# Performance work log

Measured on AMD Instinct MI355X. Metric: run time of the kernel, lower is better.

The kernel has to match this reference:

```python
import jax, jax.numpy as jnp
import numpy as np

E = 512   # embed_dim
H = 16    # num_heads
D = E // H  # head_dim = 32
L = 2048  # target (query) length
S = 2048  # source (stored pattern) length
N = 4     # batch
LN_EPS = 1e-5


def setup_inputs() -> dict:
    key = jax.random.key(0)
    ks = jax.random.split(key, 8)
    inv_sqrt_e = 1.0 / np.sqrt(E).astype(np.float32)
    return {
        "query": jax.random.normal(ks[0], (L, N, E), jnp.float32),
        "key_in": jax.random.normal(ks[1], (S, N, E), jnp.float32),
        "value": jax.random.normal(ks[2], (S, N, E), jnp.float32),
        "scaling": jax.random.uniform(ks[3], (H,), jnp.float32),  # per-head beta
        "in_proj_weight": jax.random.normal(ks[4], (3 * E, E), jnp.float32) * inv_sqrt_e,
        "in_proj_bias": jnp.zeros((3 * E,), jnp.float32),
        "p_norm_weight": jnp.ones((D,), jnp.float32),
        "p_norm_bias": jnp.zeros((D,), jnp.float32),
        "out_proj_weight": jax.random.normal(ks[5], (E, E), jnp.float32) * inv_sqrt_e,
        "out_proj_bias": jnp.zeros((E,), jnp.float32),
    }


def reference(query, key_in, value, scaling, in_proj_weight, in_proj_bias,
              p_norm_weight, p_norm_bias, out_proj_weight, out_proj_bias):
    Lq, Nb, Ed = query.shape
    Sk = key_in.shape[0]
    # split packed in-projection (torch Linear convention: y = x @ W^T + b)
    wq, wk, wv = jnp.split(in_proj_weight, 3, axis=0)
    bq, bk, bv = jnp.split(in_proj_bias, 3, axis=0)
    q = jnp.einsum('lne,fe->lnf', query, wq) + bq
    k = jnp.einsum('sne,fe->snf', key_in, wk) + bk
    v = jnp.einsum('sne,fe->snf', value, wv) + bv
    # (len, N, H*D) -> (N, H, len, D)
    q = q.reshape(Lq, Nb, H, D).transpose(1, 2, 0, 3)
    k = k.reshape(Sk, Nb, H, D).transpose(1, 2, 0, 3)
    v = v.reshape(Sk, Nb, H, D).transpose(1, 2, 0, 3)

    def pattern_norm(x):
        # affine LayerNorm over the association (head) dimension D
        mu = jnp.mean(x, axis=-1, keepdims=True)
        var = jnp.mean(jnp.square(x - mu), axis=-1, keepdims=True)
        return (x - mu) * jax.lax.rsqrt(var + LN_EPS) * p_norm_weight + p_norm_bias

    k = pattern_norm(k)
    v = pattern_norm(v)

    beta = scaling.reshape(1, H, 1, 1)  # per-head inverse-temperature
    scores = jnp.einsum('nhld,nhsd->nhls', q * beta, k)  # [N,H,L,S]
    attn = jax.nn.softmax(scores, axis=-1)  # single Hopfield update (update_steps_max=0)
    out = jnp.einsum('nhls,nhsd->nhld', attn, v)  # [N,H,L,D]
    out = out.transpose(2, 0, 1, 3).reshape(Lq, Nb, H * D)
    out = jnp.einsum('lnf,of->lno', out, out_proj_weight) + out_proj_bias
    return out  # (L, N, E)
```

## Files before the change

kernel.cpp:

```cpp
#include <hip/hip_runtime.h>
#include <cstdint>

#define LN_EPS 1e-5f

typedef _Float16 f16;
typedef _Float16 half4_t __attribute__((ext_vector_type(4)));
typedef _Float16 half8_t __attribute__((ext_vector_type(8)));
typedef __fp16 fp16v2 __attribute__((ext_vector_type(2)));
typedef float f32x4 __attribute__((ext_vector_type(4)));

__device__ __forceinline__ void gl_lds16(const void* g, void* l) {
    __builtin_amdgcn_global_load_lds(
        (__attribute__((address_space(1))) void*)(uintptr_t)g,
        (__attribute__((address_space(3))) void*)(uint32_t)(uintptr_t)l,
        16, 0, 0);
}

__device__ __forceinline__ half4_t pack4(float a, float b, float c, float d) {
    fp16v2 lo = __builtin_amdgcn_cvt_pkrtz(a, b);
    fp16v2 hi = __builtin_amdgcn_cvt_pkrtz(c, d);
    half4_t r;
    r[0] = (f16)lo[0]; r[1] = (f16)lo[1]; r[2] = (f16)hi[0]; r[3] = (f16)hi[1];
    return r;
}

__global__ void k_cast(const float* __restrict__ W1f, const float* __restrict__ W2f,
                       const float* __restrict__ Xq, const float* __restrict__ Xk,
                       const float* __restrict__ Xv,
                       f16* __restrict__ W1h, f16* __restrict__ W2h,
                       f16* __restrict__ Xh) {
    int t = blockIdx.x * blockDim.x + threadIdx.x;
    const float4* src;
    half4_t* dst;
    int idx;
    if (t < 196608)      { src = (const float4*)W1f; dst = (half4_t*)W1h; idx = t; }
    else if (t < 262144) { src = (const float4*)W2f; dst = (half4_t*)W2h; idx = t - 196608; }
    else {
        int u = t - 262144;
        int s = u >> 20;
        idx = u & 1048575;
        src = (s == 0) ? (const float4*)Xq : ((s == 1) ? (const float4*)Xk : (const float4*)Xv);
        dst = (half4_t*)(Xh + (size_t)s * 4194304);
    }
    float4 v = src[idx];
    dst[idx] = pack4(v.x, v.y, v.z, v.w);
}

__global__ __launch_bounds__(256) void k_inproj(
    const f16* __restrict__ Xh, const f16* __restrict__ W1,
    const float* __restrict__ bias, const float* __restrict__ scaling,
    f16* __restrict__ Qg, f16* __restrict__ Kg, f16* __restrict__ Vg)
{
    __shared__ __align__(16) f16 Al[128 * 32];
    __shared__ __align__(16) f16 Bl[128 * 32];

    const int tid = threadIdx.x;
    const int m0 = blockIdx.x * 128;
    const int f0 = blockIdx.y * 128;
    const int sec = f0 >> 9;
    const f16* X = Xh + (size_t)sec * 4194304;
    f16* Ob = (sec == 0) ? Qg : ((sec == 1) ? Kg : Vg);

    const int wid = tid >> 6, ln = tid & 63, l15 = ln & 15, quad = ln >> 4;
    const int wm = wid >> 1, wn = wid & 1;

    f32x4 z4 = {0.f, 0.f, 0.f, 0.f};
    f32x4 acc[4][4];
    #pragma unroll
    for (int i = 0; i < 4; ++i)
        #pragma unroll
        for (int j = 0; j < 4; ++j) acc[i][j] = z4;

    for (int kt = 0; kt < 16; ++kt) {
        const int k0 = kt * 32;
        #pragma unroll
        for (int i = 0; i < 2; ++i) {
            int row = wid * 32 + i * 16 + (ln >> 2);
            int co = (ln & 3) * 8;
            gl_lds16(W1 + (size_t)(f0 + row) * 512 + k0 + co,
                     Bl + (wid * 32 + i * 16) * 32);
            gl_lds16(X + (size_t)(m0 + row) * 512 + k0 + co,
                     Al + (wid * 32 + i * 16) * 32);
        }
        __syncthreads();

        half8_t a[4], b[4];
        #pragma unroll
        for (int i = 0; i < 4; ++i)
            a[i] = *(const half8_t*)(Al + (wm * 64 + i * 16 + l15) * 32 + quad * 8);
        #pragma unroll
        for (int j = 0; j < 4; ++j)
            b[j] = *(const half8_t*)(Bl + (wn * 64 + j * 16 + l15) * 32 + quad * 8);
        #pragma unroll
        for (int i = 0; i < 4; ++i)
            #pragma unroll
            for (int j = 0; j < 4; ++j)
                acc[i][j] = __builtin_amdgcn_mfma_f32_16x16x32_f16(b[j], a[i], acc[i][j], 0, 0, 0);
        __syncthreads();
    }

    #pragma unroll
    for (int j = 0; j < 4; ++j) {
        int fb = f0 + wn * 64 + j * 16;
        int floc = (fb & 511) + quad * 4;
        int hh = floc >> 5;
        int cc = (floc >> 3) & 3, e0 = floc & 7;
        float sc2 = (sec == 0) ? scaling[hh] * 1.44269504f : 1.0f;
        float4 bs4 = *(const float4*)(bias + fb + quad * 4);
        #pragma unroll
        for (int i = 0; i < 4; ++i) {
            int rm = m0 + wm * 64 + i * 16 + l15;
            int l = rm >> 2, nb = rm & 3;
            int gg = nb * 16 + hh;
            *(half4_t*)(Ob + (size_t)gg * 65536 + (size_t)cc * 16384 + (size_t)l * 8 + e0) =
                pack4((acc[i][j][0] + bs4.x) * sc2, (acc[i][j][1] + bs4.y) * sc2,
                      (acc[i][j][2] + bs4.z) * sc2, (acc[i][j][3] + bs4.w) * sc2);
        }
    }
}

__global__ void k_norm_kv(f16* __restrict__ Kg, const f16* __restrict__ Vg,
                          const float* __restrict__ w, const float* __restrict__ b,
                          f16* __restrict__ Vtg) {
    __shared__ __align__(16) f16 T[32 * 64];
    const int t = threadIdx.x;
    const int seg = blockIdx.x, g = blockIdx.y;
    const int s_l = t >> 2, c = t & 3;
    const size_t base = (size_t)g * 65536 + (size_t)c * 16384 + (size_t)(seg * 64 + s_l) * 8;

    half8_t kv = *(const half8_t*)(Kg + base);
    half8_t vv = *(const half8_t*)(Vg + base);
    float kf[8], vf[8];
    float ks1 = 0.f, ks2 = 0.f, vs1 = 0.f, vs2 = 0.f;
    #pragma unroll
    for (int j = 0; j < 8; ++j) {
        kf[j] = (float)kv[j]; ks1 += kf[j]; ks2 += kf[j] * kf[j];
        vf[j] = (float)vv[j]; vs1 += vf[j]; vs2 += vf[j] * vf[j];
    }
    ks1 += __shfl_xor(ks1, 1); ks1 += __shfl_xor(ks1, 2);
    ks2 += __shfl_xor(ks2, 1); ks2 += __shfl_xor(ks2, 2);
    vs1 += __shfl_xor(vs1, 1); vs1 += __shfl_xor(vs1, 2);
    vs2 += __shfl_xor(vs2, 1); vs2 += __shfl_xor(vs2, 2);
    float kmu = ks1 * (1.f / 32.f), kvar = ks2 * (1.f / 32.f) - kmu * kmu;
    float vmu = vs1 * (1.f / 32.f), vvar = vs2 * (1.f / 32.f) - vmu * vmu;
    float krs = rsqrtf(kvar + LN_EPS), vrs = rsqrtf(vvar + LN_EPS);

    half8_t ky;
    int cs = s_l >> 3, es = s_l & 7;
    #pragma unroll
    for (int j = 0; j < 8; ++j) {
        int d = c * 8 + j;
        float wd = w[d], bd = b[d];
        ky[j] = (f16)((kf[j] - kmu) * krs * wd + bd);
        T[d * 64 + (cs ^ j) * 8 + es] = (f16)((vf[j] - vmu) * vrs * wd + bd);
    }
    *(half8_t*)(Kg + base) = ky;
    __syncthreads();
    int d_o = t >> 3, c_o = t & 7;
    half8_t out = *(const half8_t*)(T + d_o * 64 + c_o * 8);
    *(half8_t*)(Vtg + (size_t)(g * 32 + seg) * 2048 + d_o * 64 + c_o * 8) = out;
}

__global__ __launch_bounds__(256, 4) void k_flash(
    const f16* __restrict__ Qg, const f16* __restrict__ Kg,
    const f16* __restrict__ Vtg, f16* __restrict__ Og)
{
    __shared__ __align__(16) char smem[40960];

    const int tid = threadIdx.x, wid = tid >> 6, ln = tid & 63;
    const int l15 = ln & 15, quad = ln >> 4, l8 = ln & 7;
    char* Pw = smem + 24576 + wid * 4096;
    const int g = blockIdx.x, h = g & 15, n = g >> 4;
    const int q0 = blockIdx.y * 128;

    half8_t aq[2];
    #pragma unroll
    for (int i = 0; i < 2; ++i)
        aq[i] = *(const half8_t*)(Qg + (size_t)g * 65536 + (size_t)quad * 16384 +
                                  (size_t)(q0 + wid * 32 + i * 16 + l15) * 8);

    const f16* kp = Kg + (size_t)g * 65536 + (size_t)wid * 16384;
    const f16* vp = Vtg + (size_t)(g * 32) * 2048 + wid * 512;
    gl_lds16(kp + (size_t)ln * 8, smem + wid * 1024);
    gl_lds16(vp + (size_t)ln * 8, smem + 12288 + wid * 1024);
    gl_lds16(kp + 512 + (size_t)ln * 8, smem + 4096 + wid * 1024);
    gl_lds16(vp + 2048 + (size_t)ln * 8, smem + 12288 + 4096 + wid * 1024);
    kp += 1024;
    vp += 4096;

    half8_t onesf;
    {
        f16 o = (l15 == 0) ? (f16)1.0f : (f16)0.0f;
        #pragma unroll
        for (int j = 0; j < 8; ++j) onesf[j] = o;
    }

    f32x4 z4 = {0.f, 0.f, 0.f, 0.f};
    f32x4 accO[2][2], accSum[2];
    accO[0][0] = z4; accO[0][1] = z4; accO[1][0] = z4; accO[1][1] = z4;
    accSum[0] = z4; accSum[1] = z4;
    float m_i[2] = {-1e30f, -1e30f};

    int cur = 0;
    for (int st = 0; st < 32; ++st) {
        if (st < 31) asm volatile("s_waitcnt vmcnt(2)" ::: "memory");
        else         asm volatile("s_waitcnt vmcnt(0)" ::: "memory");
        __builtin_amdgcn_s_barrier();

        if (st < 30) {
            int nb = cur + 2; if (nb >= 3) nb -= 3;
            gl_lds16(kp + (size_t)ln * 8, smem + nb * 4096 + wid * 1024);
            gl_lds16(vp + (size_t)ln * 8, smem + 12288 + nb * 4096 + wid * 1024);
            kp += 512;
            vp += 2048;
        }
        const char* Kl = smem + cur * 4096;
        const char* Vt = smem + 12288 + cur * 4096;

        half8_t ak[4];
        #pragma unroll
        for (int mt = 0; mt < 4; ++mt)
            ak[mt] = *(const half8_t*)(Kl + quad * 1024 + (mt * 16 + l15) * 16);
        f32x4 accS[2][4];
        __builtin_amdgcn_s_setprio(1);
        #pragma unroll
        for (int i = 0; i < 2; ++i)
            #pragma unroll
            for (int mt = 0; mt < 4; ++mt)
                accS[i][mt] = __builtin_amdgcn_mfma_f32_16x16x32_f16(ak[mt], aq[i], z4, 0, 0, 0);
        __builtin_amdgcn_s_setprio(0);

        float mn[2];
        bool up = false;
        #pragma unroll
        for (int i = 0; i < 2; ++i) {
            float xm = fmaxf(fmaxf(accS[i][0][0], accS[i][0][1]),
                             fmaxf(accS[i][0][2], accS[i][0][3]));
            #pragma unroll
            for (int mt = 1; mt < 4; ++mt)
                xm = fmaxf(xm, fmaxf(fmaxf(accS[i][mt][0], accS[i][mt][1]),
                                     fmaxf(accS[i][mt][2], accS[i][mt][3])));
            xm = fmaxf(xm, __shfl_xor(xm, 16));
            xm = fmaxf(xm, __shfl_xor(xm, 32));
            up = up || (xm > m_i[i] + 8.f);
            mn[i] = fmaxf(m_i[i], xm);
        }
        if (__ballot(up)) {
            #pragma unroll
            for (int i = 0; i < 2; ++i) {
                float alpha = __builtin_amdgcn_exp2f(m_i[i] - mn[i]);
                #pragma unroll
                for (int dt = 0; dt < 2; ++dt)
                    #pragma unroll
                    for (int r = 0; r < 4; ++r) accO[i][dt][r] *= alpha;
                #pragma unroll
                for (int r = 0; r < 4; ++r) accSum[i][r] *= alpha;
                m_i[i] = mn[i];
            }
        }

        #pragma unroll
        for (int i = 0; i < 2; ++i) {
            #pragma unroll
            for (int mt = 0; mt < 4; ++mt) {
                float p0 = __builtin_amdgcn_exp2f(accS[i][mt][0] - m_i[i]);
                float p1 = __builtin_amdgcn_exp2f(accS[i][mt][1] - m_i[i]);
                float p2 = __builtin_amdgcn_exp2f(accS[i][mt][2] - m_i[i]);
                float p3 = __builtin_amdgcn_exp2f(accS[i][mt][3] - m_i[i]);
                int ch = (mt * 2 + (quad >> 1)) ^ l8;
                *(half4_t*)(Pw + (i * 16 + l15) * 128 + ch * 16 + (quad & 1) * 8) =
                    pack4(p0, p1, p2, p3);
            }
        }

        #pragma unroll
        for (int kt = 0; kt < 2; ++kt) {
            half8_t av[2], bp[2];
            #pragma unroll
            for (int dt = 0; dt < 2; ++dt) {
                int d = dt * 16 + l15;
                int cp = (kt * 4 + quad) ^ (l15 & 7);
                av[dt] = *(const half8_t*)(Vt + d * 128 + cp * 16);
            }
            #pragma unroll
            for (int i = 0; i < 2; ++i)
                bp[i] = *(const half8_t*)(Pw + (i * 16 + l15) * 128 +
                                          (((kt * 4 + quad) ^ l8) * 16));
            __builtin_amdgcn_s_setprio(1);
            #pragma unroll
            for (int i = 0; i < 2; ++i) {
                #pragma unroll
                for (int dt = 0; dt < 2; ++dt)
                    accO[i][dt] = __builtin_amdgcn_mfma_f32_16x16x32_f16(av[dt], bp[i], accO[i][dt], 0, 0, 0);
                accSum[i] = __builtin_amdgcn_mfma_f32_16x16x32_f16(onesf, bp[i], accSum[i], 0, 0, 0);
            }
            __builtin_amdgcn_s_setprio(0);
        }

        cur = cur + 1; if (cur == 3) cur = 0;
    }

    #pragma unroll
    for (int i = 0; i < 2; ++i) {
        float li = __shfl(accSum[i][0], l15);
        float inv = 1.f / li;
        #pragma unroll
        for (int dt = 0; dt < 2; ++dt)
            *(half4_t*)(Pw + (i * 16 + l15) * 80 + (dt * 16 + quad * 4) * 2) =
                pack4(accO[i][dt][0] * inv, accO[i][dt][1] * inv,
                      accO[i][dt][2] * inv, accO[i][dt][3] * inv);
    }
    int q2 = ln >> 1, hf = ln & 1;
    half8_t o0 = *(const half8_t*)(Pw + q2 * 80 + hf * 32);
    half8_t o1 = *(const half8_t*)(Pw + q2 * 80 + hf * 32 + 16);
    size_t rowe = ((size_t)(n * 2048 + q0 + wid * 32 + q2)) * 512 + h * 32 + hf * 16;
    *(half8_t*)(Og + rowe) = o0;
    *(half8_t*)(Og + rowe + 8) = o1;
}

__global__ __launch_bounds__(256) void k_outproj(
    const f16* __restrict__ A, const f16* __restrict__ W2,
    const float* __restrict__ bias, float* __restrict__ Out)
{
    __shared__ __align__(16) f16 Al[128 * 32];
    __shared__ __align__(16) f16 Bl[128 * 32];

    const int tid = threadIdx.x;
    const int m0 = blockIdx.x * 128;
    const int f0 = blockIdx.y * 128;
    const int wid = tid >> 6, ln = tid & 63, l15 = ln & 15, quad = ln >> 4;
    const int wm = wid >> 1, wn = wid & 1;

    f32x4 z4 = {0.f, 0.f, 0.f, 0.f};
    f32x4 acc[4][4];
    #pragma unroll
    for (int i = 0; i < 4; ++i)
        #pragma unroll
        for (int j = 0; j < 4; ++j) acc[i][j] = z4;

    for (int kt = 0; kt < 16; ++kt) {
        const int k0 = kt * 32;
        #pragma unroll
        for (int i = 0; i < 2; ++i) {
            int row = wid * 32 + i * 16 + (ln >> 2);
            gl_lds16(A + (size_t)(m0 + row) * 512 + k0 + (ln & 3) * 8,
                     Al + (wid * 32 + i * 16) * 32);
            gl_lds16(W2 + (size_t)(f0 + row) * 512 + k0 + (ln & 3) * 8,
                     Bl + (wid * 32 + i * 16) * 32);
        }
        __syncthreads();

        half8_t a[4], b[4];
        #pragma unroll
        for (int i = 0; i < 4; ++i)
            a[i] = *(const half8_t*)(Al + (wm * 64 + i * 16 + l15) * 32 + quad * 8);
        #pragma unroll
        for (int j = 0; j < 4; ++j)
            b[j] = *(const half8_t*)(Bl + (wn * 64 + j * 16 + l15) * 32 + quad * 8);
        #pragma unroll
        for (int i = 0; i < 4; ++i)
            #pragma unroll
            for (int j = 0; j < 4; ++j)
                acc[i][j] = __builtin_amdgcn_mfma_f32_16x16x32_f16(b[j], a[i], acc[i][j], 0, 0, 0);
        __syncthreads();
    }

    #pragma unroll
    for (int j = 0; j < 4; ++j) {
        int fb = f0 + wn * 64 + j * 16;
        float4 bs4 = *(const float4*)(bias + fb + quad * 4);
        #pragma unroll
        for (int i = 0; i < 4; ++i) {
            int rm = m0 + wm * 64 + i * 16 + l15;
            int orow = (rm & 2047) * 4 + (rm >> 11);
            float4 o;
            o.x = acc[i][j][0] + bs4.x;
            o.y = acc[i][j][1] + bs4.y;
            o.z = acc[i][j][2] + bs4.z;
            o.w = acc[i][j][3] + bs4.w;
            *(float4*)(Out + (size_t)orow * 512 + fb + quad * 4) = o;
        }
    }
}

extern "C" void kernel_launch(void* const* d_in, const int* in_sizes, int n_in,
                              void* d_out, int out_size, void* d_ws, size_t ws_size,
                              hipStream_t stream) {
    const float* query   = (const float*)d_in[0];
    const float* key_in  = (const float*)d_in[1];
    const float* value   = (const float*)d_in[2];
    const float* scaling = (const float*)d_in[3];
    const float* ipw     = (const float*)d_in[4];
    const float* ipb     = (const float*)d_in[5];
    const float* pnw     = (const float*)d_in[6];
    const float* pnb     = (const float*)d_in[7];
    const float* opw     = (const float*)d_in[8];
    const float* opb     = (const float*)d_in[9];
    float* out = (float*)d_out;

    f16* Qg  = (f16*)d_ws;
    f16* Kg  = Qg + (size_t)4194304;
    f16* Vg  = Qg + (size_t)8388608;
    f16* W1  = Qg + (size_t)12582912;
    f16* W2  = Qg + (size_t)13369344;
    f16* Xh  = Qg + (size_t)13631488;
    f16* Vtg = Xh;
    f16* Og  = Vg;

    k_cast<<<13312, 256, 0, stream>>>(ipw, opw, query, key_in, value, W1, W2, Xh);
    k_inproj<<<dim3(64, 12), 256, 0, stream>>>(Xh, W1, ipb, scaling, Qg, Kg, Vg);
    k_norm_kv<<<dim3(32, 64), 256, 0, stream>>>(Kg, Vg, pnw, pnb, Vtg);
    k_flash<<<dim3(64, 16), 256, 0, stream>>>(Qg, Kg, Vtg, Og);
    k_outproj<<<dim3(64, 4), 256, 0, stream>>>(Og, W2, opb, out);
}
```

Baseline: 220.7 us.

## Software-pipeline QK^T one tile ahead of softmax and PV in flash loop

Restructures the flash-attention main loop so the score MFMAs for the next K tile are issued before the softmax and PV work of the current tile. Two score register sets ping-pong through a manually unrolled pair of loop bodies, and the wait count is tightened to match. Occupancy is lowered from 4 to 3 blocks per SM to make room for the extra live accumulators. The aim is to overlap MFMA latency with exp/softmax VALU work, at the cost of more registers and fewer resident waves.

```diff
diff --git a/kernel.cpp b/kernel.cpp
--- a/kernel.cpp
+++ b/kernel.cpp
@@ -161,7 +161,7 @@
     *(half8_t*)(Vtg + (size_t)(g * 32 + seg) * 2048 + d_o * 64 + c_o * 8) = out;
 }
 
-__global__ __launch_bounds__(256, 4) void k_flash(
+__global__ __launch_bounds__(256, 3) void k_flash(
     const f16* __restrict__ Qg, const f16* __restrict__ Kg,
     const f16* __restrict__ Vtg, f16* __restrict__ Og)
 {
@@ -172,12 +172,6 @@
     char* Pw = smem + 24576 + wid * 4096;
     const int g = blockIdx.x, h = g & 15, n = g >> 4;
     const int q0 = blockIdx.y * 128;
-
-    half8_t aq[2];
-    #pragma unroll
-    for (int i = 0; i < 2; ++i)
-        aq[i] = *(const half8_t*)(Qg + (size_t)g * 65536 + (size_t)quad * 16384 +
-                                  (size_t)(q0 + wid * 32 + i * 16 + l15) * 8);
 
     const f16* kp = Kg + (size_t)g * 65536 + (size_t)wid * 16384;
     const f16* vp = Vtg + (size_t)(g * 32) * 2048 + wid * 512;
@@ -188,6 +182,12 @@
     kp += 1024;
     vp += 4096;
 
+    half8_t aq[2];
+    #pragma unroll
+    for (int i = 0; i < 2; ++i)
+        aq[i] = *(const half8_t*)(Qg + (size_t)g * 65536 + (size_t)quad * 16384 +
+                                  (size_t)(q0 + wid * 32 + i * 16 + l15) * 8);
+
     half8_t onesf;
     {
         f16 o = (l15 == 0) ? (f16)1.0f : (f16)0.0f;
@@ -201,45 +201,62 @@
     accSum[0] = z4; accSum[1] = z4;
     float m_i[2] = {-1e30f, -1e30f};
 
+    asm volatile("s_waitcnt vmcnt(0)" ::: "memory");
+    __builtin_amdgcn_s_barrier();
+
+    f32x4 S0[2][4], S1[2][4];
+    {
+        half8_t ak[4];
+        #pragma unroll
+        for (int mt = 0; mt < 4; ++mt)
+            ak[mt] = *(const half8_t*)(smem + quad * 1024 + (mt * 16 + l15) * 16);
+        #pragma unroll
+        for (int i = 0; i < 2; ++i)
+            #pragma unroll
+            for (int mt = 0; mt < 4; ++mt)
+                S0[i][mt] = __builtin_amdgcn_mfma_f32_16x16x32_f16(ak[mt], aq[i], z4, 0, 0, 0);
+    }
+
     int cur = 0;
-    for (int st = 0; st < 32; ++st) {
-        if (st < 31) asm volatile("s_waitcnt vmcnt(2)" ::: "memory");
+    auto body = [&](f32x4 (&SC)[2][4], f32x4 (&SN)[2][4], int st) {
+        if (st < 31) asm volatile("s_waitcnt vmcnt(1)" ::: "memory");
         else         asm volatile("s_waitcnt vmcnt(0)" ::: "memory");
         __builtin_amdgcn_s_barrier();
 
-        if (st < 30) {
+        if (st <= 29) {
             int nb = cur + 2; if (nb >= 3) nb -= 3;
             gl_lds16(kp + (size_t)ln * 8, smem + nb * 4096 + wid * 1024);
             gl_lds16(vp + (size_t)ln * 8, smem + 12288 + nb * 4096 + wid * 1024);
             kp += 512;
             vp += 2048;
         }
-        const char* Kl = smem + cur * 4096;
-        const char* Vt = smem + 12288 + cur * 4096;
-
-        half8_t ak[4];
-        #pragma unroll
-        for (int mt = 0; mt < 4; ++mt)
-            ak[mt] = *(const half8_t*)(Kl + quad * 1024 + (mt * 16 + l15) * 16);
-        f32x4 accS[2][4];
-        __builtin_amdgcn_s_setprio(1);
-        #pragma unroll
-        for (int i = 0; i < 2; ++i)
+
+        if (st <= 30) {
+            int nx = cur + 1; if (nx >= 3) nx -= 3;
+            const char* Kn = smem + nx * 4096;
+            half8_t ak[4];
             #pragma unroll
             for (int mt = 0; mt < 4; ++mt)
-                accS[i][mt] = __builtin_amdgcn_mfma_f32_16x16x32_f16(ak[mt], aq[i], z4, 0, 0, 0);
-        __builtin_amdgcn_s_setprio(0);
+                ak[mt] = *(const half8_t*)(Kn + quad * 1024 + (mt * 16 + l15) * 16);
+            __builtin_amdgcn_s_setprio(1);
+            #pragma unroll
+            for (int i = 0; i < 2; ++i)
+                #pragma unroll
+                for (int mt = 0; mt < 4; ++mt)
+                    SN[i][mt] = __builtin_amdgcn_mfma_f32_16x16x32_f16(ak[mt], aq[i], z4, 0, 0, 0);
+            __builtin_amdgcn_s_setprio(0);
+        }
 
         float mn[2];
         bool up = false;
         #pragma unroll
         for (int i = 0; i < 2; ++i) {
-            float xm = fmaxf(fmaxf(accS[i][0][0], accS[i][0][1]),
-                             fmaxf(accS[i][0][2], accS[i][0][3]));
+            float xm = fmaxf(fmaxf(SC[i][0][0], SC[i][0][1]),
+                             fmaxf(SC[i][0][2], SC[i][0][3]));
             #pragma unroll
             for (int mt = 1; mt < 4; ++mt)
-                xm = fmaxf(xm, fmaxf(fmaxf(accS[i][mt][0], accS[i][mt][1]),
-                                     fmaxf(accS[i][mt][2], accS[i][mt][3])));
+                xm = fmaxf(xm, fmaxf(fmaxf(SC[i][mt][0], SC[i][mt][1]),
+                                     fmaxf(SC[i][mt][2], SC[i][mt][3])));
             xm = fmaxf(xm, __shfl_xor(xm, 16));
             xm = fmaxf(xm, __shfl_xor(xm, 32));
             up = up || (xm > m_i[i] + 8.f);
@@ -263,16 +280,17 @@
         for (int i = 0; i < 2; ++i) {
             #pragma unroll
             for (int mt = 0; mt < 4; ++mt) {
-                float p0 = __builtin_amdgcn_exp2f(accS[i][mt][0] - m_i[i]);
-                float p1 = __builtin_amdgcn_exp2f(accS[i][mt][1] - m_i[i]);
-                float p2 = __builtin_amdgcn_exp2f(accS[i][mt][2] - m_i[i]);
-                float p3 = __builtin_amdgcn_exp2f(accS[i][mt][3] - m_i[i]);
+                float p0 = __builtin_amdgcn_exp2f(SC[i][mt][0] - m_i[i]);
+                float p1 = __builtin_amdgcn_exp2f(SC[i][mt][1] - m_i[i]);
+                float p2 = __builtin_amdgcn_exp2f(SC[i][mt][2] - m_i[i]);
+                float p3 = __builtin_amdgcn_exp2f(SC[i][mt][3] - m_i[i]);
                 int ch = (mt * 2 + (quad >> 1)) ^ l8;
                 *(half4_t*)(Pw + (i * 16 + l15) * 128 + ch * 16 + (quad & 1) * 8) =
                     pack4(p0, p1, p2, p3);
             }
         }
 
+        const char* Vt = smem + 12288 + cur * 4096;
         #pragma unroll
         for (int kt = 0; kt < 2; ++kt) {
             half8_t av[2], bp[2];
@@ -298,6 +316,11 @@
         }
 
         cur = cur + 1; if (cur == 3) cur = 0;
+    };
+
+    for (int it = 0; it < 16; ++it) {
+        body(S0, S1, it * 2);
+        body(S1, S0, it * 2 + 1);
     }
 
     #pragma unroll
```

Result: slower. 232.7 us (+5.4%).

## Triple-buffer LDS loads in projection GEMMs and halve outproj M tile

Applied to the files above, without the earlier changes.

Both projection GEMMs now use a three-slot LDS ring with async global-to-LDS loads issued two k-steps ahead. Explicit vmcnt waits and a single barrier per iteration replace the two __syncthreads, and s_setprio is raised around the MFMA block so memory latency overlaps with compute. The output projection also shrinks its M tile from 128 to 64 rows, doubling its grid to 512 blocks so more CUs are busy. The cost is more LDS per block and reliance on hand-counted vmcnt values, which are fragile if the compiler reorders or adds memory ops.

```diff
diff --git a/kernel.cpp b/kernel.cpp
--- a/kernel.cpp
+++ b/kernel.cpp
@@ -51,8 +51,8 @@
     const float* __restrict__ bias, const float* __restrict__ scaling,
     f16* __restrict__ Qg, f16* __restrict__ Kg, f16* __restrict__ Vg)
 {
-    __shared__ __align__(16) f16 Al[128 * 32];
-    __shared__ __align__(16) f16 Bl[128 * 32];
+    __shared__ __align__(16) f16 Al[3][128 * 32];
+    __shared__ __align__(16) f16 Bl[3][128 * 32];
 
     const int tid = threadIdx.x;
     const int m0 = blockIdx.x * 128;
@@ -63,6 +63,7 @@
 
     const int wid = tid >> 6, ln = tid & 63, l15 = ln & 15, quad = ln >> 4;
     const int wm = wid >> 1, wn = wid & 1;
+    const int srow = ln >> 2, sco = (ln & 3) * 8;
 
     f32x4 z4 = {0.f, 0.f, 0.f, 0.f};
     f32x4 acc[4][4];
@@ -71,32 +72,47 @@
         #pragma unroll
         for (int j = 0; j < 4; ++j) acc[i][j] = z4;
 
+    auto issue = [&](int kt, int slot) {
+        const int k0 = kt * 32;
+        #pragma unroll
+        for (int i = 0; i < 2; ++i) {
+            int row = wid * 32 + i * 16 + srow;
+            gl_lds16(W1 + (size_t)(f0 + row) * 512 + k0 + sco,
+                     Bl[slot] + (wid * 32 + i * 16) * 32);
+            gl_lds16(X + (size_t)(m0 + row) * 512 + k0 + sco,
+                     Al[slot] + (wid * 32 + i * 16) * 32);
+        }
+    };
+    issue(0, 0);
+    issue(1, 1);
+
+    int slot = 0;
     for (int kt = 0; kt < 16; ++kt) {
-        const int k0 = kt * 32;
-        #pragma unroll
-        for (int i = 0; i < 2; ++i) {
-            int row = wid * 32 + i * 16 + (ln >> 2);
-            int co = (ln & 3) * 8;
-            gl_lds16(W1 + (size_t)(f0 + row) * 512 + k0 + co,
-                     Bl + (wid * 32 + i * 16) * 32);
-            gl_lds16(X + (size_t)(m0 + row) * 512 + k0 + co,
-                     Al + (wid * 32 + i * 16) * 32);
-        }
-        __syncthreads();
+        if (kt < 15) asm volatile("s_waitcnt vmcnt(4)" ::: "memory");
+        else         asm volatile("s_waitcnt vmcnt(0)" ::: "memory");
+        __builtin_amdgcn_s_barrier();
+
+        if (kt < 14) {
+            int nb = slot + 2; if (nb >= 3) nb -= 3;
+            issue(kt + 2, nb);
+        }
 
         half8_t a[4], b[4];
         #pragma unroll
         for (int i = 0; i < 4; ++i)
-            a[i] = *(const half8_t*)(Al + (wm * 64 + i * 16 + l15) * 32 + quad * 8);
+            a[i] = *(const half8_t*)(Al[slot] + (wm * 64 + i * 16 + l15) * 32 + quad * 8);
         #pragma unroll
         for (int j = 0; j < 4; ++j)
-            b[j] = *(const half8_t*)(Bl + (wn * 64 + j * 16 + l15) * 32 + quad * 8);
+            b[j] = *(const half8_t*)(Bl[slot] + (wn * 64 + j * 16 + l15) * 32 + quad * 8);
+        __builtin_amdgcn_s_setprio(1);
         #pragma unroll
         for (int i = 0; i < 4; ++i)
             #pragma unroll
             for (int j = 0; j < 4; ++j)
                 acc[i][j] = __builtin_amdgcn_mfma_f32_16x16x32_f16(b[j], a[i], acc[i][j], 0, 0, 0);
-        __syncthreads();
+        __builtin_amdgcn_s_setprio(0);
+
+        slot = slot + 1; if (slot == 3) slot = 0;
     }
 
     #pragma unroll
@@ -322,47 +338,65 @@
     const f16* __restrict__ A, const f16* __restrict__ W2,
     const float* __restrict__ bias, float* __restrict__ Out)
 {
-    __shared__ __align__(16) f16 Al[128 * 32];
-    __shared__ __align__(16) f16 Bl[128 * 32];
+    __shared__ __align__(16) f16 Al[3][64 * 32];
+    __shared__ __align__(16) f16 Bl[3][128 * 32];
 
     const int tid = threadIdx.x;
-    const int m0 = blockIdx.x * 128;
+    const int m0 = blockIdx.x * 64;
     const int f0 = blockIdx.y * 128;
     const int wid = tid >> 6, ln = tid & 63, l15 = ln & 15, quad = ln >> 4;
     const int wm = wid >> 1, wn = wid & 1;
+    const int srow = ln >> 2, sco = (ln & 3) * 8;
 
     f32x4 z4 = {0.f, 0.f, 0.f, 0.f};
-    f32x4 acc[4][4];
-    #pragma unroll
-    for (int i = 0; i < 4; ++i)
+    f32x4 acc[2][4];
+    #pragma unroll
+    for (int i = 0; i < 2; ++i)
         #pragma unroll
         for (int j = 0; j < 4; ++j) acc[i][j] = z4;
 
+    auto issue = [&](int kt, int slot) {
+        const int k0 = kt * 32;
+        int arow = wid * 16 + srow;
+        gl_lds16(A + (size_t)(m0 + arow) * 512 + k0 + sco,
+                 Al[slot] + wid * 512);
+        #pragma unroll
+        for (int i = 0; i < 2; ++i) {
+            int brow = wid * 32 + i * 16 + srow;
+            gl_lds16(W2 + (size_t)(f0 + brow) * 512 + k0 + sco,
+                     Bl[slot] + (wid * 32 + i * 16) * 32);
+        }
+    };
+    issue(0, 0);
+    issue(1, 1);
+
+    int slot = 0;
     for (int kt = 0; kt < 16; ++kt) {
-        const int k0 = kt * 32;
-        #pragma unroll
-        for (int i = 0; i < 2; ++i) {
-            int row = wid * 32 + i * 16 + (ln >> 2);
-            gl_lds16(A + (size_t)(m0 + row) * 512 + k0 + (ln & 3) * 8,
-                     Al + (wid * 32 + i * 16) * 32);
-            gl_lds16(W2 + (size_t)(f0 + row) * 512 + k0 + (ln & 3) * 8,
-                     Bl + (wid * 32 + i * 16) * 32);
-        }
-        __syncthreads();
-
-        half8_t a[4], b[4];
-        #pragma unroll
-        for (int i = 0; i < 4; ++i)
-            a[i] = *(const half8_t*)(Al + (wm * 64 + i * 16 + l15) * 32 + quad * 8);
+        if (kt < 15) asm volatile("s_waitcnt vmcnt(3)" ::: "memory");
+        else         asm volatile("s_waitcnt vmcnt(0)" ::: "memory");
+        __builtin_amdgcn_s_barrier();
+
+        if (kt < 14) {
+            int nb = slot + 2; if (nb >= 3) nb -= 3;
+            issue(kt + 2, nb);
+        }
+
+        half8_t a[2], b[4];
+        #pragma unroll
+        for (int i = 0; i < 2; ++i)
+            a[i] = *(const half8_t*)(Al[slot] + (wm * 32 + i * 16 + l15) * 32 + quad * 8);
         #pragma unroll
         for (int j = 0; j < 4; ++j)
-            b[j] = *(const half8_t*)(Bl + (wn * 64 + j * 16 + l15) * 32 + quad * 8);
-        #pragma unroll
-        for (int i = 0; i < 4; ++i)
+            b[j] = *(const half8_t*)(Bl[slot] + (wn * 64 + j * 16 + l15) * 32 + quad * 8);
+        __builtin_amdgcn_s_setprio(1);
+        #pragma unroll
+        for (int i = 0; i < 2; ++i)
             #pragma unroll
             for (int j = 0; j < 4; ++j)
                 acc[i][j] = __builtin_amdgcn_mfma_f32_16x16x32_f16(b[j], a[i], acc[i][j], 0, 0, 0);
-        __syncthreads();
+        __builtin_amdgcn_s_setprio(0);
+
+        slot = slot + 1; if (slot == 3) slot = 0;
     }
 
     #pragma unroll
@@ -370,8 +404,8 @@
         int fb = f0 + wn * 64 + j * 16;
         float4 bs4 = *(const float4*)(bias + fb + quad * 4);
         #pragma unroll
-        for (int i = 0; i < 4; ++i) {
-            int rm = m0 + wm * 64 + i * 16 + l15;
+        for (int i = 0; i < 2; ++i) {
+            int rm = m0 + wm * 32 + i * 16 + l15;
             int orow = (rm & 2047) * 4 + (rm >> 11);
             float4 o;
             o.x = acc[i][j][0] + bs4.x;
@@ -411,5 +445,5 @@
     k_inproj<<<dim3(64, 12), 256, 0, stream>>>(Xh, W1, ipb, scaling, Qg, Kg, Vg);
     k_norm_kv<<<dim3(32, 64), 256, 0, stream>>>(Kg, Vg, pnw, pnb, Vtg);
     k_flash<<<dim3(64, 16), 256, 0, stream>>>(Qg, Kg, Vtg, Og);
-    k_outproj<<<dim3(64, 4), 256, 0, stream>>>(Og, W2, opb, out);
-}
+    k_outproj<<<dim3(128, 4), 256, 0, stream>>>(Og, W2, opb, out);
+}
```

Result: faster. 213.0 us (-3.5%).
